# Performance work log

Measured on AMD Instinct MI355X. Metric: run time of the kernel, lower is better.

Reference implementation:

```python
import jax, jax.numpy as jnp
import numpy as np

B, N, IN, HID, H, OUT = 32, 512, 64, 64, 4, 64
NEG_SLOPE = 0.2
NEG_INF = -1e9


def setup_inputs() -> dict:
    key = jax.random.key(0)
    ks = jax.random.split(key, 10)
    s = 0.1
    return {
        "x": jax.random.normal(ks[0], (B, N, IN), jnp.float32),
        "adj": jax.random.randint(ks[1], (B, N, N), 0, 2, jnp.int32),
        "W1": jax.random.normal(ks[2], (IN, H * HID), jnp.float32) * s,
        "a1_src": jax.random.normal(ks[3], (H, HID), jnp.float32) * s,
        "a1_dst": jax.random.normal(ks[4], (H, HID), jnp.float32) * s,
        "b1": jnp.zeros((H * HID,), jnp.float32),
        "W2": jax.random.normal(ks[5], (H * HID, OUT), jnp.float32) * s,
        "a2_src": jax.random.normal(ks[6], (1, OUT), jnp.float32) * s,
        "a2_dst": jax.random.normal(ks[7], (1, OUT), jnp.float32) * s,
        "b2": jnp.zeros((OUT,), jnp.float32),
    }


def _gat_layer(x, mask, W, a_src, a_dst, b, heads, feat):
    # x: [N, Fin]; mask: [N_dst, N_src] bool (edge src->dst), self-loops included
    h = (x @ W).reshape(N, heads, feat)              # [N, H, F]
    e_src = jnp.einsum('nhf,hf->nh', h, a_src)       # [N, H]
    e_dst = jnp.einsum('nhf,hf->nh', h, a_dst)       # [N, H]
    # scores[d, s, h] = leaky_relu(a_dst.x_d + a_src.x_s)
    scores = jax.nn.leaky_relu(e_dst[:, None, :] + e_src[None, :, :], NEG_SLOPE)
    scores = jnp.where(mask[:, :, None], scores, NEG_INF)
    alpha = jax.nn.softmax(scores, axis=1)           # segment-softmax over src neighbors
    out = jnp.einsum('dsh,shf->dhf', alpha, h)       # aggregate messages
    return out.reshape(N, heads * feat) + b


def reference(x, adj, W1, a1_src, a1_dst, b1, W2, a2_src, a2_dst, b2):
    eye = jnp.eye(N, dtype=bool)

    def one_graph(xi, ai):
        # edge i->j when adj[i, j] != 0 (coo row=src, col=dst); add self-loops
        mask = (ai != 0).T | eye                     # [dst, src]
        h1 = jax.nn.elu(_gat_layer(xi, mask, W1, a1_src, a1_dst, b1, H, HID))
        return _gat_layer(h1, mask, W2, a2_src, a2_dst, b2, 1, OUT)

    return jax.vmap(one_graph)(x, adj)               # [B, N, OUT]
```

## Files before the change

kernel.cpp:

```cpp
#include <hip/hip_runtime.h>
#include <cstddef>

#define NN 512
#define NEG_SLOPE 0.2f

typedef __attribute__((ext_vector_type(8))) short short8;
typedef __attribute__((ext_vector_type(16))) float f32x16;

__device__ __forceinline__ unsigned short f2bf(float v) {
  unsigned u = __float_as_uint(v);
  return (unsigned short)((u + 0x7FFFu + ((u >> 16) & 1u)) >> 16);
}

__global__ __launch_bounds__(256) void k_prep(const float* __restrict__ W1,
                                              const float* __restrict__ W2,
                                              short8* __restrict__ W1B,
                                              short8* __restrict__ W2B) {
  int blk = blockIdx.x, t = threadIdx.x;
  if (blk < 8) {
    int idx = blk * 256 + t;
    int unit = idx >> 6, lane = idx & 63;
    int nt = unit >> 2, kt = unit & 3;
    int f = nt * 32 + (lane & 31);
    int k0 = kt * 16 + ((lane >> 5) << 3);
    short8 r;
#pragma unroll
    for (int j = 0; j < 8; ++j) r[j] = (short)f2bf(W1[(k0 + j) * 256 + f]);
    W1B[idx] = r;
  } else {
    int idx = (blk - 8) * 256 + t;
    int unit = idx >> 6, lane = idx & 63;
    int nt = unit >> 4, kt = unit & 15;
    int f = nt * 32 + (lane & 31);
    int k0 = kt * 16 + ((lane >> 5) << 3);
    short8 r;
#pragma unroll
    for (int j = 0; j < 8; ++j) r[j] = (short)f2bf(W2[(k0 + j) * 64 + f]);
    W2B[idx] = r;
  }
}

__global__ __launch_bounds__(256) void k_g1m(const int* __restrict__ adj,
                                             const float* __restrict__ x,
                                             const short8* __restrict__ W1B,
                                             const float* __restrict__ a1s,
                                             const float* __restrict__ a1d,
                                             unsigned* __restrict__ mask,
                                             unsigned short* __restrict__ hb1,
                                             float* __restrict__ e1s,
                                             float* __restrict__ e1d) {
  __shared__ float tile[32 * 36];
  int i = blockIdx.x;
  int b = (i & 7) * 4 + ((i >> 3) & 3), mt = i >> 5;
  int d0 = mt * 32;
  int t = threadIdx.x;

  if (t >= 64) {
    int t2 = t - 64;
    const int* abase = adj + (size_t)b * NN * NN;
    for (int u = t2; u < 512; u += 192) {
      int d = d0 + (u & 31), w = u >> 5;
      unsigned wv = 0;
#pragma unroll
      for (int j = 0; j < 32; ++j) {
        int s = w * 32 + j;
        unsigned bit = ((abase[(size_t)s * NN + d] != 0) || (s == d)) ? 1u : 0u;
        wv |= bit << j;
      }
      mask[((size_t)b * 16 + w) * NN + d] = wv;
    }
    return;
  }

  int lane = t, m = lane & 31, kg = lane >> 5;
  const float* xrow = x + ((size_t)b * NN + d0 + m) * 64 + kg * 8;
  short8 a[4];
#pragma unroll
  for (int kt = 0; kt < 4; ++kt) {
    float4 v0 = *(const float4*)(xrow + kt * 16);
    float4 v1 = *(const float4*)(xrow + kt * 16 + 4);
    short8 r;
    r[0] = (short)f2bf(v0.x); r[1] = (short)f2bf(v0.y);
    r[2] = (short)f2bf(v0.z); r[3] = (short)f2bf(v0.w);
    r[4] = (short)f2bf(v1.x); r[5] = (short)f2bf(v1.y);
    r[6] = (short)f2bf(v1.z); r[7] = (short)f2bf(v1.w);
    a[kt] = r;
  }
  short8* hb8 = (short8*)hb1;
  short8 wf[2][4];
#pragma unroll
  for (int kt = 0; kt < 4; ++kt) wf[0][kt] = W1B[kt * 64 + lane];
  float e_h = 0.f;
#pragma unroll
  for (int nt = 0; nt < 8; ++nt) {
    int cur = nt & 1;
    if (nt < 7) {
#pragma unroll
      for (int kt = 0; kt < 4; ++kt)
        wf[cur ^ 1][kt] = W1B[((nt + 1) * 4 + kt) * 64 + lane];
    }
    f32x16 acc;
#pragma unroll
    for (int q = 0; q < 16; ++q) acc[q] = 0.f;
#pragma unroll
    for (int kt = 0; kt < 4; ++kt)
      acc = __builtin_amdgcn_mfma_f32_32x32x16_bf16(a[kt], wf[cur][kt], acc, 0, 0, 0);
#pragma unroll
    for (int reg = 0; reg < 16; ++reg) {
      int row = (reg & 3) + 8 * (reg >> 2) + 4 * kg;
      tile[row * 36 + m] = acc[reg];
    }
    int h = nt >> 1, ft = nt & 1;
#pragma unroll
    for (int ktl = 0; ktl < 2; ++ktl) {
      short8 r;
#pragma unroll
      for (int j = 0; j < 8; ++j)
        r[j] = (short)f2bf(tile[(ktl * 16 + kg * 8 + j) * 36 + m]);
      hb8[((((size_t)b * 4 + h) * 32 + mt * 2 + ktl) * 2 + ft) * 64 + lane] = r;
    }
    const float* coeff = (kg ? a1d : a1s) + h * 64 + ft * 32;
    float ep = 0.f;
#pragma unroll
    for (int c4 = 0; c4 < 8; ++c4) {
      float4 tv = *(const float4*)&tile[m * 36 + c4 * 4];
      float4 cv = *(const float4*)&coeff[c4 * 4];
      ep += tv.x * cv.x + tv.y * cv.y + tv.z * cv.z + tv.w * cv.w;
    }
    e_h += ep;
    if (ft) {
      float* p = kg ? e1d : e1s;
      p[((size_t)b * 4 + h) * NN + d0 + m] = e_h;
      e_h = 0.f;
    }
  }
}

__global__ __launch_bounds__(256) void k_attn1g2(const unsigned* __restrict__ mask,
                                                 const unsigned short* __restrict__ hb1,
                                                 const float* __restrict__ e1s,
                                                 const float* __restrict__ e1d,
                                                 const float* __restrict__ b1,
                                                 const short8* __restrict__ W2B,
                                                 const float* __restrict__ a2s,
                                                 const float* __restrict__ a2d,
                                                 unsigned short* __restrict__ hb2,
                                                 float* __restrict__ e2s,
                                                 float* __restrict__ e2d) {
  __shared__ float es[4 * NN];
  __shared__ unsigned mw[16 * 32];
  __shared__ unsigned short ht[32 * 264];
  __shared__ float tile2[2][32 * 36];
  int i = blockIdx.x;
  int b = (i & 7) * 4 + ((i >> 3) & 3), mt = i >> 5;
  int d0 = mt * 32;
  int t = threadIdx.x;
  const float* esrc = e1s + (size_t)b * 4 * NN;
#pragma unroll
  for (int q = 0; q < 8; ++q) es[t + q * 256] = esrc[t + q * 256];
  const unsigned* msrc = mask + (size_t)b * 16 * NN + d0;
  mw[t] = msrc[(t >> 5) * NN + (t & 31)];
  {
    int idx = t + 256;
    mw[idx] = msrc[(idx >> 5) * NN + (idx & 31)];
  }
  __syncthreads();
  int h = t >> 6, lane = t & 63, m = lane & 31, kg = lane >> 5;
  float ed = e1d[((size_t)b * 4 + h) * NN + d0 + m];
  const short8* bfr = (const short8*)hb1 + ((size_t)b * 4 + h) * 32 * 2 * 64;
  f32x16 acc0, acc1;
#pragma unroll
  for (int q = 0; q < 16; ++q) { acc0[q] = 0.f; acc1[q] = 0.f; }
  float l = 0.f;
  for (int kt = 0; kt < 32; ++kt) {
    unsigned wv = mw[(kt >> 1) * 32 + m];
    int shift = (kt & 1) * 16 + kg * 8;
    const float* ep = &es[h * NN + kt * 16 + kg * 8];
    short8 a;
#pragma unroll
    for (int j = 0; j < 8; ++j) {
      float sc = ed + ep[j];
      sc = fmaxf(sc, NEG_SLOPE * sc);
      float pv = __expf(sc);
      pv = ((wv >> (shift + j)) & 1u) ? pv : 0.f;
      l += pv;
      a[j] = (short)f2bf(pv);
    }
    short8 bv0 = bfr[(kt * 2 + 0) * 64 + lane];
    short8 bv1 = bfr[(kt * 2 + 1) * 64 + lane];
    acc0 = __builtin_amdgcn_mfma_f32_32x32x16_bf16(a, bv0, acc0, 0, 0, 0);
    acc1 = __builtin_amdgcn_mfma_f32_32x32x16_bf16(a, bv1, acc1, 0, 0, 0);
  }
  float lf = l + __shfl(l, lane ^ 32, 64);
  float linv = 1.f / lf;
  float bia0 = b1[h * 64 + m];
  float bia1 = b1[h * 64 + 32 + m];
#pragma unroll
  for (int reg = 0; reg < 16; ++reg) {
    int row = (reg & 3) + 8 * (reg >> 2) + 4 * kg;
    float li = __shfl(linv, row, 64);
    float v0 = acc0[reg] * li + bia0;
    v0 = (v0 > 0.f) ? v0 : (__expf(v0) - 1.f);
    float v1 = acc1[reg] * li + bia1;
    v1 = (v1 > 0.f) ? v1 : (__expf(v1) - 1.f);
    ht[row * 264 + h * 64 + m] = f2bf(v0);
    ht[row * 264 + h * 64 + 32 + m] = f2bf(v1);
  }
  __syncthreads();
  int w2 = t >> 6;
  if (w2 < 2) {
    int nt = w2;
    short8 wfr[16];
#pragma unroll
    for (int kt = 0; kt < 16; ++kt) wfr[kt] = W2B[(nt * 16 + kt) * 64 + lane];
    f32x16 acc;
#pragma unroll
    for (int q = 0; q < 16; ++q) acc[q] = 0.f;
#pragma unroll
    for (int kt = 0; kt < 16; ++kt) {
      short8 av = *(const short8*)&ht[m * 264 + kt * 16 + kg * 8];
      acc = __builtin_amdgcn_mfma_f32_32x32x16_bf16(av, wfr[kt], acc, 0, 0, 0);
    }
    float* tw = tile2[nt];
#pragma unroll
    for (int reg = 0; reg < 16; ++reg) {
      int row = (reg & 3) + 8 * (reg >> 2) + 4 * kg;
      tw[row * 36 + m] = acc[reg];
    }
  }
  __syncthreads();
  if (w2 < 2) {
    const float* tw = tile2[w2];
    short8* hb8 = (short8*)hb2;
#pragma unroll
    for (int ktl = 0; ktl < 2; ++ktl) {
      short8 r;
#pragma unroll
      for (int j = 0; j < 8; ++j)
        r[j] = (short)f2bf(tw[(ktl * 16 + kg * 8 + j) * 36 + m]);
      hb8[(((size_t)b * 32 + mt * 2 + ktl) * 2 + w2) * 64 + lane] = r;
    }
  } else {
    const float* coeff = ((w2 == 2) ? a2s : a2d) + kg * 32;
    const float* tsrc = tile2[kg];
    float val = 0.f;
#pragma unroll
    for (int c4 = 0; c4 < 8; ++c4) {
      float4 tv = *(const float4*)&tsrc[m * 36 + c4 * 4];
      float4 cv = *(const float4*)&coeff[c4 * 4];
      val += tv.x * cv.x + tv.y * cv.y + tv.z * cv.z + tv.w * cv.w;
    }
    float tot = val + __shfl(val, lane ^ 32, 64);
    if (kg == 0) {
      float* p = (w2 == 2) ? e2s : e2d;
      p[(size_t)b * NN + d0 + m] = tot;
    }
  }
}

__global__ __launch_bounds__(256) void k_attn2(const unsigned* __restrict__ mask,
                                               const unsigned short* __restrict__ hb2,
                                               const float* __restrict__ e2s,
                                               const float* __restrict__ e2d,
                                               const float* __restrict__ b2,
                                               float* __restrict__ out) {
  __shared__ float es[NN];
  __shared__ unsigned mw[16 * 32];
  __shared__ float cred[4][2][16][64];
  __shared__ float lred[4][64];
  __shared__ float linv_s[32];
  int i = blockIdx.x;
  int b = (i & 7) * 4 + ((i >> 3) & 3);
  int d0 = (i >> 5) * 32;
  int t = threadIdx.x;
  es[t] = e2s[(size_t)b * NN + t];
  es[t + 256] = e2s[(size_t)b * NN + t + 256];
  const unsigned* msrc = mask + (size_t)b * 16 * NN + d0;
  mw[t] = msrc[(t >> 5) * NN + (t & 31)];
  {
    int idx = t + 256;
    mw[idx] = msrc[(idx >> 5) * NN + (idx & 31)];
  }
  __syncthreads();
  int w = t >> 6, lane = t & 63, m = lane & 31, kg = lane >> 5;
  float ed = e2d[(size_t)b * NN + d0 + m];
  const short8* bfr = (const short8*)hb2 + (size_t)b * 32 * 2 * 64;
  f32x16 acc0, acc1;
#pragma unroll
  for (int q = 0; q < 16; ++q) { acc0[q] = 0.f; acc1[q] = 0.f; }
  float l = 0.f;
#pragma unroll
  for (int kk = 0; kk < 8; ++kk) {
    int kt = w * 8 + kk;
    unsigned wv = mw[(kt >> 1) * 32 + m];
    int shift = (kt & 1) * 16 + kg * 8;
    const float* ep = &es[kt * 16 + kg * 8];
    short8 a;
#pragma unroll
    for (int j = 0; j < 8; ++j) {
      float sc = ed + ep[j];
      sc = fmaxf(sc, NEG_SLOPE * sc);
      float pv = __expf(sc);
      pv = ((wv >> (shift + j)) & 1u) ? pv : 0.f;
      l += pv;
      a[j] = (short)f2bf(pv);
    }
    short8 bv0 = bfr[(kt * 2 + 0) * 64 + lane];
    short8 bv1 = bfr[(kt * 2 + 1) * 64 + lane];
    acc0 = __builtin_amdgcn_mfma_f32_32x32x16_bf16(a, bv0, acc0, 0, 0, 0);
    acc1 = __builtin_amdgcn_mfma_f32_32x32x16_bf16(a, bv1, acc1, 0, 0, 0);
  }
  lred[w][lane] = l;
#pragma unroll
  for (int reg = 0; reg < 16; ++reg) {
    cred[w][0][reg][lane] = acc0[reg];
    cred[w][1][reg][lane] = acc1[reg];
  }
  __syncthreads();
  if (t < 32) {
    float s = 0.f;
#pragma unroll
    for (int q = 0; q < 4; ++q) s += lred[q][t] + lred[q][t + 32];
    linv_s[t] = 1.f / s;
  }
  __syncthreads();
#pragma unroll
  for (int q = 0; q < 8; ++q) {
    int pos = t + q * 256;
    int nt = pos >> 10;
    int rem = pos & 1023;
    int reg = rem >> 6;
    int ln = rem & 63;
    float v = cred[0][nt][reg][ln] + cred[1][nt][reg][ln] +
              cred[2][nt][reg][ln] + cred[3][nt][reg][ln];
    int row = (reg & 3) + 8 * (reg >> 2) + 4 * (ln >> 5);
    int col = nt * 32 + (ln & 31);
    out[((size_t)b * NN + d0 + row) * 64 + col] = v * linv_s[row] + b2[col];
  }
}

extern "C" void kernel_launch(void* const* d_in, const int* in_sizes, int n_in,
                              void* d_out, int out_size, void* d_ws, size_t ws_size,
                              hipStream_t stream) {
  const float* x = (const float*)d_in[0];
  const int* adj = (const int*)d_in[1];
  const float* W1 = (const float*)d_in[2];
  const float* a1s = (const float*)d_in[3];
  const float* a1d = (const float*)d_in[4];
  const float* b1 = (const float*)d_in[5];
  const float* W2 = (const float*)d_in[6];
  const float* a2s = (const float*)d_in[7];
  const float* a2d = (const float*)d_in[8];
  const float* b2 = (const float*)d_in[9];
  float* out = (float*)d_out;

  char* w = (char*)d_ws;
  unsigned* mask = (unsigned*)w;
  short8* W1B = (short8*)(w + (3u << 20));
  short8* W2B = (short8*)(w + (3u << 20) + (64u << 10));
  unsigned short* hb1 = (unsigned short*)(w + (4u << 20));
  float* e1s = (float*)(w + (12u << 20));
  float* e1d = (float*)(w + (12u << 20) + (256u << 10));
  unsigned short* hb2 = (unsigned short*)(w + (21u << 20));
  float* e2s = (float*)(w + (23u << 20));
  float* e2d = (float*)(w + (23u << 20) + (64u << 10));

  hipLaunchKernelGGL(k_prep, dim3(16), dim3(256), 0, stream, W1, W2, W1B, W2B);
  hipLaunchKernelGGL(k_g1m, dim3(512), dim3(256), 0, stream, adj, x, W1B, a1s,
                     a1d, mask, hb1, e1s, e1d);
  hipLaunchKernelGGL(k_attn1g2, dim3(512), dim3(256), 0, stream, mask, hb1,
                     e1s, e1d, b1, W2B, a2s, a2d, hb2, e2s, e2d);
  hipLaunchKernelGGL(k_attn2, dim3(512), dim3(256), 0, stream, mask, hb2, e2s,
                     e2d, b2, out);
}
```

Before: 123.1 us.

## Fuse three GAT phases into one cooperative kernel with grid-wide syncs

```diff
diff --git a/kernel.cpp b/kernel.cpp
--- a/kernel.cpp
+++ b/kernel.cpp
@@ -1,5 +1,8 @@
 #include <hip/hip_runtime.h>
+#include <hip/hip_cooperative_groups.h>
 #include <cstddef>
+
+namespace cg = cooperative_groups;
 
 #define NN 512
 #define NEG_SLOPE 0.2f
@@ -40,26 +43,24 @@
   }
 }
 
-__global__ __launch_bounds__(256) void k_g1m(const int* __restrict__ adj,
-                                             const float* __restrict__ x,
-                                             const short8* __restrict__ W1B,
-                                             const float* __restrict__ a1s,
-                                             const float* __restrict__ a1d,
-                                             unsigned* __restrict__ mask,
-                                             unsigned short* __restrict__ hb1,
-                                             float* __restrict__ e1s,
-                                             float* __restrict__ e1d) {
-  __shared__ float tile[32 * 36];
-  int i = blockIdx.x;
+__device__ __forceinline__ void phase1(int i, int t, char* smem,
+                                       const int* __restrict__ adj,
+                                       const float* __restrict__ x,
+                                       const short8* __restrict__ W1B,
+                                       const float* __restrict__ a1s,
+                                       const float* __restrict__ a1d,
+                                       unsigned* __restrict__ mask,
+                                       unsigned short* __restrict__ hb1,
+                                       float* __restrict__ e1s,
+                                       float* __restrict__ e1d) {
   int b = (i & 7) * 4 + ((i >> 3) & 3), mt = i >> 5;
   int d0 = mt * 32;
-  int t = threadIdx.x;
-
   if (t >= 64) {
     int t2 = t - 64;
     const int* abase = adj + (size_t)b * NN * NN;
     for (int u = t2; u < 512; u += 192) {
-      int d = d0 + (u & 31), w = u >> 5;
+      int dl = u & 31, w = u >> 5;
+      int d = d0 + dl;
       unsigned wv = 0;
 #pragma unroll
       for (int j = 0; j < 32; ++j) {
@@ -69,101 +70,97 @@
       }
       mask[((size_t)b * 16 + w) * NN + d] = wv;
     }
-    return;
-  }
-
-  int lane = t, m = lane & 31, kg = lane >> 5;
-  const float* xrow = x + ((size_t)b * NN + d0 + m) * 64 + kg * 8;
-  short8 a[4];
-#pragma unroll
-  for (int kt = 0; kt < 4; ++kt) {
-    float4 v0 = *(const float4*)(xrow + kt * 16);
-    float4 v1 = *(const float4*)(xrow + kt * 16 + 4);
-    short8 r;
-    r[0] = (short)f2bf(v0.x); r[1] = (short)f2bf(v0.y);
-    r[2] = (short)f2bf(v0.z); r[3] = (short)f2bf(v0.w);
-    r[4] = (short)f2bf(v1.x); r[5] = (short)f2bf(v1.y);
-    r[6] = (short)f2bf(v1.z); r[7] = (short)f2bf(v1.w);
-    a[kt] = r;
-  }
-  short8* hb8 = (short8*)hb1;
-  short8 wf[2][4];
-#pragma unroll
-  for (int kt = 0; kt < 4; ++kt) wf[0][kt] = W1B[kt * 64 + lane];
-  float e_h = 0.f;
-#pragma unroll
-  for (int nt = 0; nt < 8; ++nt) {
-    int cur = nt & 1;
-    if (nt < 7) {
+  } else {
+    float* tile = (float*)smem;
+    int lane = t, m = lane & 31, kg = lane >> 5;
+    const float* xrow = x + ((size_t)b * NN + d0 + m) * 64 + kg * 8;
+    short8 a[4];
+#pragma unroll
+    for (int kt = 0; kt < 4; ++kt) {
+      float4 v0 = *(const float4*)(xrow + kt * 16);
+      float4 v1 = *(const float4*)(xrow + kt * 16 + 4);
+      short8 r;
+      r[0] = (short)f2bf(v0.x); r[1] = (short)f2bf(v0.y);
+      r[2] = (short)f2bf(v0.z); r[3] = (short)f2bf(v0.w);
+      r[4] = (short)f2bf(v1.x); r[5] = (short)f2bf(v1.y);
+      r[6] = (short)f2bf(v1.z); r[7] = (short)f2bf(v1.w);
+      a[kt] = r;
+    }
+    short8* hb8 = (short8*)hb1;
+    short8 wf[2][4];
+#pragma unroll
+    for (int kt = 0; kt < 4; ++kt) wf[0][kt] = W1B[kt * 64 + lane];
+    float e_h = 0.f;
+#pragma unroll
+    for (int nt = 0; nt < 8; ++nt) {
+      int cur = nt & 1;
+      if (nt < 7) {
+#pragma unroll
+        for (int kt = 0; kt < 4; ++kt)
+          wf[cur ^ 1][kt] = W1B[((nt + 1) * 4 + kt) * 64 + lane];
+      }
+      f32x16 acc;
+#pragma unroll
+      for (int q = 0; q < 16; ++q) acc[q] = 0.f;
 #pragma unroll
       for (int kt = 0; kt < 4; ++kt)
-        wf[cur ^ 1][kt] = W1B[((nt + 1) * 4 + kt) * 64 + lane];
-    }
-    f32x16 acc;
-#pragma unroll
-    for (int q = 0; q < 16; ++q) acc[q] = 0.f;
-#pragma unroll
-    for (int kt = 0; kt < 4; ++kt)
-      acc = __builtin_amdgcn_mfma_f32_32x32x16_bf16(a[kt], wf[cur][kt], acc, 0, 0, 0);
-#pragma unroll
-    for (int reg = 0; reg < 16; ++reg) {
-      int row = (reg & 3) + 8 * (reg >> 2) + 4 * kg;
-      tile[row * 36 + m] = acc[reg];
-    }
-    int h = nt >> 1, ft = nt & 1;
-#pragma unroll
-    for (int ktl = 0; ktl < 2; ++ktl) {
-      short8 r;
-#pragma unroll
-      for (int j = 0; j < 8; ++j)
-        r[j] = (short)f2bf(tile[(ktl * 16 + kg * 8 + j) * 36 + m]);
-      hb8[((((size_t)b * 4 + h) * 32 + mt * 2 + ktl) * 2 + ft) * 64 + lane] = r;
-    }
-    const float* coeff = (kg ? a1d : a1s) + h * 64 + ft * 32;
-    float ep = 0.f;
-#pragma unroll
-    for (int c4 = 0; c4 < 8; ++c4) {
-      float4 tv = *(const float4*)&tile[m * 36 + c4 * 4];
-      float4 cv = *(const float4*)&coeff[c4 * 4];
-      ep += tv.x * cv.x + tv.y * cv.y + tv.z * cv.z + tv.w * cv.w;
-    }
-    e_h += ep;
-    if (ft) {
-      float* p = kg ? e1d : e1s;
-      p[((size_t)b * 4 + h) * NN + d0 + m] = e_h;
-      e_h = 0.f;
-    }
-  }
-}
-
-__global__ __launch_bounds__(256) void k_attn1g2(const unsigned* __restrict__ mask,
-                                                 const unsigned short* __restrict__ hb1,
-                                                 const float* __restrict__ e1s,
-                                                 const float* __restrict__ e1d,
-                                                 const float* __restrict__ b1,
-                                                 const short8* __restrict__ W2B,
-                                                 const float* __restrict__ a2s,
-                                                 const float* __restrict__ a2d,
-                                                 unsigned short* __restrict__ hb2,
-                                                 float* __restrict__ e2s,
-                                                 float* __restrict__ e2d) {
-  __shared__ float es[4 * NN];
-  __shared__ unsigned mw[16 * 32];
-  __shared__ unsigned short ht[32 * 264];
-  __shared__ float tile2[2][32 * 36];
-  int i = blockIdx.x;
+        acc = __builtin_amdgcn_mfma_f32_32x32x16_bf16(a[kt], wf[cur][kt], acc, 0, 0, 0);
+#pragma unroll
+      for (int reg = 0; reg < 16; ++reg) {
+        int row = (reg & 3) + 8 * (reg >> 2) + 4 * kg;
+        tile[row * 36 + m] = acc[reg];
+      }
+      int h = nt >> 1, ft = nt & 1;
+#pragma unroll
+      for (int ktl = 0; ktl < 2; ++ktl) {
+        short8 r;
+#pragma unroll
+        for (int j = 0; j < 8; ++j)
+          r[j] = (short)f2bf(tile[(ktl * 16 + kg * 8 + j) * 36 + m]);
+        hb8[((((size_t)b * 4 + h) * 32 + mt * 2 + ktl) * 2 + ft) * 64 + lane] = r;
+      }
+      const float* coeff = (kg ? a1d : a1s) + h * 64 + ft * 32;
+      float ep = 0.f;
+#pragma unroll
+      for (int c4 = 0; c4 < 8; ++c4) {
+        float4 tv = *(const float4*)&tile[m * 36 + c4 * 4];
+        float4 cv = *(const float4*)&coeff[c4 * 4];
+        ep += tv.x * cv.x + tv.y * cv.y + tv.z * cv.z + tv.w * cv.w;
+      }
+      e_h += ep;
+      if (ft) {
+        float* p = kg ? e1d : e1s;
+        p[((size_t)b * 4 + h) * NN + d0 + m] = e_h;
+        e_h = 0.f;
+      }
+    }
+  }
+}
+
+__device__ __forceinline__ void phase2(int i, int t, char* smem,
+                                       const unsigned* __restrict__ mask,
+                                       const unsigned short* __restrict__ hb1,
+                                       const float* __restrict__ e1s,
+                                       const float* __restrict__ e1d,
+                                       const float* __restrict__ b1,
+                                       const short8* __restrict__ W2B,
+                                       const float* __restrict__ a2s,
+                                       const float* __restrict__ a2d,
+                                       unsigned short* __restrict__ hb2,
+                                       float* __restrict__ e2s,
+                                       float* __restrict__ e2d) {
+  float* es = (float*)smem;
+  unsigned* mw = (unsigned*)(smem + 8192);
+  unsigned short* ht = (unsigned short*)(smem + 10240);
+  float* tile2 = (float*)(smem + 27136);
   int b = (i & 7) * 4 + ((i >> 3) & 3), mt = i >> 5;
   int d0 = mt * 32;
-  int t = threadIdx.x;
   const float* esrc = e1s + (size_t)b * 4 * NN;
 #pragma unroll
   for (int q = 0; q < 8; ++q) es[t + q * 256] = esrc[t + q * 256];
   const unsigned* msrc = mask + (size_t)b * 16 * NN + d0;
   mw[t] = msrc[(t >> 5) * NN + (t & 31)];
-  {
-    int idx = t + 256;
-    mw[idx] = msrc[(idx >> 5) * NN + (idx & 31)];
-  }
+  mw[t + 256] = msrc[((t + 256) >> 5) * NN + (t & 31)];
   __syncthreads();
   int h = t >> 6, lane = t & 63, m = lane & 31, kg = lane >> 5;
   float ed = e1d[((size_t)b * 4 + h) * NN + d0 + m];
@@ -221,7 +218,7 @@
       short8 av = *(const short8*)&ht[m * 264 + kt * 16 + kg * 8];
       acc = __builtin_amdgcn_mfma_f32_32x32x16_bf16(av, wfr[kt], acc, 0, 0, 0);
     }
-    float* tw = tile2[nt];
+    float* tw = tile2 + nt * 1152;
 #pragma unroll
     for (int reg = 0; reg < 16; ++reg) {
       int row = (reg & 3) + 8 * (reg >> 2) + 4 * kg;
@@ -230,7 +227,7 @@
   }
   __syncthreads();
   if (w2 < 2) {
-    const float* tw = tile2[w2];
+    const float* tw = tile2 + w2 * 1152;
     short8* hb8 = (short8*)hb2;
 #pragma unroll
     for (int ktl = 0; ktl < 2; ++ktl) {
@@ -242,7 +239,7 @@
     }
   } else {
     const float* coeff = ((w2 == 2) ? a2s : a2d) + kg * 32;
-    const float* tsrc = tile2[kg];
+    const float* tsrc = tile2 + kg * 1152;
     float val = 0.f;
 #pragma unroll
     for (int c4 = 0; c4 < 8; ++c4) {
@@ -258,29 +255,25 @@
   }
 }
 
-__global__ __launch_bounds__(256) void k_attn2(const unsigned* __restrict__ mask,
-                                               const unsigned short* __restrict__ hb2,
-                                               const float* __restrict__ e2s,
-                                               const float* __restrict__ e2d,
-                                               const float* __restrict__ b2,
-                                               float* __restrict__ out) {
-  __shared__ float es[NN];
-  __shared__ unsigned mw[16 * 32];
-  __shared__ float cred[4][2][16][64];
-  __shared__ float lred[4][64];
-  __shared__ float linv_s[32];
-  int i = blockIdx.x;
+__device__ __forceinline__ void phase3(int i, int t, char* smem,
+                                       const unsigned* __restrict__ mask,
+                                       const unsigned short* __restrict__ hb2,
+                                       const float* __restrict__ e2s,
+                                       const float* __restrict__ e2d,
+                                       const float* __restrict__ b2,
+                                       float* __restrict__ out) {
+  float* es2 = (float*)smem;
+  unsigned* mw = (unsigned*)(smem + 2048);
+  float* cred = (float*)(smem + 4096);
+  float* lred = (float*)(smem + 36864);
+  float* linvs = (float*)(smem + 37888);
   int b = (i & 7) * 4 + ((i >> 3) & 3);
   int d0 = (i >> 5) * 32;
-  int t = threadIdx.x;
-  es[t] = e2s[(size_t)b * NN + t];
-  es[t + 256] = e2s[(size_t)b * NN + t + 256];
+  es2[t] = e2s[(size_t)b * NN + t];
+  es2[t + 256] = e2s[(size_t)b * NN + t + 256];
   const unsigned* msrc = mask + (size_t)b * 16 * NN + d0;
   mw[t] = msrc[(t >> 5) * NN + (t & 31)];
-  {
-    int idx = t + 256;
-    mw[idx] = msrc[(idx >> 5) * NN + (idx & 31)];
-  }
+  mw[t + 256] = msrc[((t + 256) >> 5) * NN + (t & 31)];
   __syncthreads();
   int w = t >> 6, lane = t & 63, m = lane & 31, kg = lane >> 5;
   float ed = e2d[(size_t)b * NN + d0 + m];
@@ -294,7 +287,7 @@
     int kt = w * 8 + kk;
     unsigned wv = mw[(kt >> 1) * 32 + m];
     int shift = (kt & 1) * 16 + kg * 8;
-    const float* ep = &es[kt * 16 + kg * 8];
+    const float* ep = &es2[kt * 16 + kg * 8];
     short8 a;
 #pragma unroll
     for (int j = 0; j < 8; ++j) {
@@ -310,18 +303,18 @@
     acc0 = __builtin_amdgcn_mfma_f32_32x32x16_bf16(a, bv0, acc0, 0, 0, 0);
     acc1 = __builtin_amdgcn_mfma_f32_32x32x16_bf16(a, bv1, acc1, 0, 0, 0);
   }
-  lred[w][lane] = l;
+  lred[w * 64 + lane] = l;
 #pragma unroll
   for (int reg = 0; reg < 16; ++reg) {
-    cred[w][0][reg][lane] = acc0[reg];
-    cred[w][1][reg][lane] = acc1[reg];
+    cred[((w * 2 + 0) * 16 + reg) * 64 + lane] = acc0[reg];
+    cred[((w * 2 + 1) * 16 + reg) * 64 + lane] = acc1[reg];
   }
   __syncthreads();
   if (t < 32) {
     float s = 0.f;
 #pragma unroll
-    for (int q = 0; q < 4; ++q) s += lred[q][t] + lred[q][t + 32];
-    linv_s[t] = 1.f / s;
+    for (int q = 0; q < 4; ++q) s += lred[q * 64 + t] + lred[q * 64 + t + 32];
+    linvs[t] = 1.f / s;
   }
   __syncthreads();
 #pragma unroll
@@ -331,12 +324,69 @@
     int rem = pos & 1023;
     int reg = rem >> 6;
     int ln = rem & 63;
-    float v = cred[0][nt][reg][ln] + cred[1][nt][reg][ln] +
-              cred[2][nt][reg][ln] + cred[3][nt][reg][ln];
+    float v = cred[((0 * 2 + nt) * 16 + reg) * 64 + ln] +
+              cred[((1 * 2 + nt) * 16 + reg) * 64 + ln] +
+              cred[((2 * 2 + nt) * 16 + reg) * 64 + ln] +
+              cred[((3 * 2 + nt) * 16 + reg) * 64 + ln];
     int row = (reg & 3) + 8 * (reg >> 2) + 4 * (ln >> 5);
     int col = nt * 32 + (ln & 31);
-    out[((size_t)b * NN + d0 + row) * 64 + col] = v * linv_s[row] + b2[col];
-  }
+    out[((size_t)b * NN + d0 + row) * 64 + col] = v * linvs[row] + b2[col];
+  }
+}
+
+__global__ __launch_bounds__(256, 2) void k_mega(
+    const int* __restrict__ adj, const float* __restrict__ x,
+    const short8* __restrict__ W1B, const float* __restrict__ a1s,
+    const float* __restrict__ a1d, const float* __restrict__ b1,
+    const short8* __restrict__ W2B, const float* __restrict__ a2s,
+    const float* __restrict__ a2d, const float* __restrict__ b2,
+    unsigned* __restrict__ mask, unsigned short* __restrict__ hb1,
+    float* __restrict__ e1s, float* __restrict__ e1d,
+    unsigned short* __restrict__ hb2, float* __restrict__ e2s,
+    float* __restrict__ e2d, float* __restrict__ out) {
+  __shared__ __align__(16) char smem[38016];
+  cg::grid_group grid = cg::this_grid();
+  int i = blockIdx.x, t = threadIdx.x;
+  phase1(i, t, smem, adj, x, W1B, a1s, a1d, mask, hb1, e1s, e1d);
+  grid.sync();
+  phase2(i, t, smem, mask, hb1, e1s, e1d, b1, W2B, a2s, a2d, hb2, e2s, e2d);
+  grid.sync();
+  phase3(i, t, smem, mask, hb2, e2s, e2d, b2, out);
+}
+
+__global__ __launch_bounds__(256) void k_p1(const int* __restrict__ adj,
+                                            const float* __restrict__ x,
+                                            const short8* __restrict__ W1B,
+                                            const float* __restrict__ a1s,
+                                            const float* __restrict__ a1d,
+                                            unsigned* __restrict__ mask,
+                                            unsigned short* __restrict__ hb1,
+                                            float* __restrict__ e1s,
+                                            float* __restrict__ e1d) {
+  __shared__ __align__(16) char smem[4608];
+  phase1(blockIdx.x, threadIdx.x, smem, adj, x, W1B, a1s, a1d, mask, hb1, e1s, e1d);
+}
+
+__global__ __launch_bounds__(256) void k_p2(
+    const unsigned* __restrict__ mask, const unsigned short* __restrict__ hb1,
+    const float* __restrict__ e1s, const float* __restrict__ e1d,
+    const float* __restrict__ b1, const short8* __restrict__ W2B,
+    const float* __restrict__ a2s, const float* __restrict__ a2d,
+    unsigned short* __restrict__ hb2, float* __restrict__ e2s,
+    float* __restrict__ e2d) {
+  __shared__ __align__(16) char smem[36352];
+  phase2(blockIdx.x, threadIdx.x, smem, mask, hb1, e1s, e1d, b1, W2B, a2s, a2d,
+         hb2, e2s, e2d);
+}
+
+__global__ __launch_bounds__(256) void k_p3(const unsigned* __restrict__ mask,
+                                            const unsigned short* __restrict__ hb2,
+                                            const float* __restrict__ e2s,
+                                            const float* __restrict__ e2d,
+                                            const float* __restrict__ b2,
+                                            float* __restrict__ out) {
+  __shared__ __align__(16) char smem[38016];
+  phase3(blockIdx.x, threadIdx.x, smem, mask, hb2, e2s, e2d, b2, out);
 }
 
 extern "C" void kernel_launch(void* const* d_in, const int* in_sizes, int n_in,
@@ -355,21 +405,33 @@
   float* out = (float*)d_out;
 
   char* w = (char*)d_ws;
-  unsigned* mask = (unsigned*)w;
-  short8* W1B = (short8*)(w + (3u << 20));
-  short8* W2B = (short8*)(w + (3u << 20) + (64u << 10));
-  unsigned short* hb1 = (unsigned short*)(w + (4u << 20));
+  short8* W1B = (short8*)w;
+  short8* W2B = (short8*)(w + (64u << 10));
+  unsigned* mask = (unsigned*)(w + (128u << 10));
+  unsigned short* hb1 = (unsigned short*)(w + (2u << 20));
   float* e1s = (float*)(w + (12u << 20));
   float* e1d = (float*)(w + (12u << 20) + (256u << 10));
-  unsigned short* hb2 = (unsigned short*)(w + (21u << 20));
-  float* e2s = (float*)(w + (23u << 20));
-  float* e2d = (float*)(w + (23u << 20) + (64u << 10));
+  unsigned short* hb2 = (unsigned short*)(w + (16u << 20));
+  float* e2s = (float*)(w + (20u << 20));
+  float* e2d = (float*)(w + (20u << 20) + (64u << 10));
 
   hipLaunchKernelGGL(k_prep, dim3(16), dim3(256), 0, stream, W1, W2, W1B, W2B);
-  hipLaunchKernelGGL(k_g1m, dim3(512), dim3(256), 0, stream, adj, x, W1B, a1s,
-                     a1d, mask, hb1, e1s, e1d);
-  hipLaunchKernelGGL(k_attn1g2, dim3(512), dim3(256), 0, stream, mask, hb1,
-                     e1s, e1d, b1, W2B, a2s, a2d, hb2, e2s, e2d);
-  hipLaunchKernelGGL(k_attn2, dim3(512), dim3(256), 0, stream, mask, hb2, e2s,
-                     e2d, b2, out);
-}
+
+  void* args[18];
+  args[0] = (void*)&adj;   args[1] = (void*)&x;    args[2] = (void*)&W1B;
+  args[3] = (void*)&a1s;   args[4] = (void*)&a1d;  args[5] = (void*)&b1;
+  args[6] = (void*)&W2B;   args[7] = (void*)&a2s;  args[8] = (void*)&a2d;
+  args[9] = (void*)&b2;    args[10] = (void*)&mask; args[11] = (void*)&hb1;
+  args[12] = (void*)&e1s;  args[13] = (void*)&e1d; args[14] = (void*)&hb2;
+  args[15] = (void*)&e2s;  args[16] = (void*)&e2d; args[17] = (void*)&out;
+  hipError_t err = hipLaunchCooperativeKernel((const void*)k_mega, dim3(512),
+                                              dim3(256), args, 0, stream);
+  if (err != hipSuccess) {
+    hipLaunchKernelGGL(k_p1, dim3(512), dim3(256), 0, stream, adj, x, W1B, a1s,
+                       a1d, mask, hb1, e1s, e1d);
+    hipLaunchKernelGGL(k_p2, dim3(512), dim3(256), 0, stream, mask, hb1, e1s,
+                       e1d, b1, W2B, a2s, a2d, hb2, e2s, e2d);
+    hipLaunchKernelGGL(k_p3, dim3(512), dim3(256), 0, stream, mask, hb2, e2s,
+                       e2d, b2, out);
+  }
+}
```

Measured after the change: 254.2 us. 106% more time.
